# Optimization experiments

Hardware: AMD Instinct MI355X
Metric: run time of the kernel (lower is better)

Reference implementation:

```python
import jax, jax.numpy as jnp
import numpy as np
from math import gcd


def _get_start_index(length):
    if length <= 2:
        return 0
    return (length - 1) // 2


def setup_inputs() -> dict:
    key = jax.random.key(0)
    k1, k2 = jax.random.split(key)
    N = 8388608          # signal length (2^23 samples)
    F = 1023             # FIR taps
    x = jax.random.normal(k1, (N,), dtype=jnp.float32)
    filter_coeffs = jax.random.normal(k2, (F,), dtype=jnp.float32)
    return {"x": x, "up": 3, "down": 2, "filter_coeffs": filter_coeffs}


def reference(x, up, down, filter_coeffs):
    # Reduce the rational ratio (static Python ints)
    g = gcd(up, down)
    up = up // g
    down = down // g

    N = x.shape[0]
    F = filter_coeffs.shape[0]

    # Zero-stuff: x_up[::up] = up * x  -> length up*N
    x_up = jnp.zeros(up * N, dtype=x.dtype).at[::up].set(up * x)

    start = _get_start_index(F)
    out_len = (N * up) // down + bool((N * up) % down)

    if up == 1 and down == 1:
        return x_up[:out_len]

    # torch.conv1d(x_up, flip(h), padding=F-1) == full convolution np.convolve(x_up, h)
    full = jnp.convolve(x_up, filter_coeffs, mode="full")  # length up*N + F - 1
    x_out = full[start::down]
    return x_out[:out_len]
```

## Files before the change

### kernel.cpp

```cpp
#include <hip/hip_runtime.h>


typedef __attribute__((ext_vector_type(8))) short bf16x8;
typedef __attribute__((ext_vector_type(4))) float f32x4;

constexpr int SBLK = 4096;
constexpr int TPW  = 4;
constexpr int NQ   = 12;
constexpr int XSEG = 1072;
constexpr int AFN  = 3 * NQ * 64;

__device__ __forceinline__ unsigned short f2bf(float f) {
    union { float f; unsigned int u; } c; c.f = f;
    unsigned int u = c.u;
    return (unsigned short)((u + 0x7FFFu + ((u >> 16) & 1u)) >> 16);
}
__device__ __forceinline__ int swz(int seg) { return seg ^ ((seg >> 3) & 7); }

__global__ __launch_bounds__(256)
void build_afr_kernel(const float* __restrict__ h, uint4* __restrict__ afr)
{
    const int e = blockIdx.x * 256 + threadIdx.x;
    if (e >= AFN) return;
    const int r   = e / 768;
    const int rem = e - r * 768;
    const int q   = rem >> 6;
    const int le  = rem & 63;
    const int Tb  = 32 * q + 2 * (le & 15) + 8 * (le >> 4);
    unsigned int w[4];
    #pragma unroll
    for (int jp = 0; jp < 4; ++jp) {
        unsigned short half[2];
        #pragma unroll
        for (int u = 0; u < 2; ++u) {
            const int t   = Tb + 2 * jp + u - 32;
            const int hix = (r == 0) ? 3 * t - 2 : ((r == 1) ? 3 * t : 3 * t + 2);
            half[u] = (t >= 0 && hix >= 0 && hix < 1023) ? f2bf(3.0f * h[hix])
                                                         : (unsigned short)0;
        }
        w[jp] = (unsigned)half[0] | ((unsigned)half[1] << 16);
    }
    afr[e] = make_uint4(w[0], w[1], w[2], w[3]);
}

__global__ __launch_bounds__(256)
void resample_mfma_kernel(const float* __restrict__ x,
                          const uint4* __restrict__ afr,
                          float* __restrict__ out, int N)
{
    __shared__ __align__(16) unsigned short xr[8576];

    const int tid = threadIdx.x;
    const int s0  = blockIdx.x * SBLK;
    const int GHI = 2 * s0 + 8363;

    for (int st = tid; st < XSEG; st += 256) {
        const int g7 = GHI - 8 * st - 7;
        float f[8];
        if (g7 >= 0 && g7 + 7 < N) {
            const float4 lo = *reinterpret_cast<const float4*>(x + g7);
            const float4 hi = *reinterpret_cast<const float4*>(x + g7 + 4);
            f[0] = hi.w; f[1] = hi.z; f[2] = hi.y; f[3] = hi.x;
            f[4] = lo.w; f[5] = lo.z; f[6] = lo.y; f[7] = lo.x;
        } else {
            #pragma unroll
            for (int e = 0; e < 8; ++e) {
                const int idx = GHI - 8 * st - e;
                f[e] = (idx >= 0 && idx < N) ? x[idx] : 0.0f;
            }
        }
        uint4 w;
        w.x = (unsigned)f2bf(f[0]) | ((unsigned)f2bf(f[1]) << 16);
        w.y = (unsigned)f2bf(f[2]) | ((unsigned)f2bf(f[3]) << 16);
        w.z = (unsigned)f2bf(f[4]) | ((unsigned)f2bf(f[5]) << 16);
        w.w = (unsigned)f2bf(f[6]) | ((unsigned)f2bf(f[7]) << 16);
        *reinterpret_cast<uint4*>(xr + 8 * swz(st)) = w;
    }
    __syncthreads();

    const int wave = tid >> 6;
    const int lane = tid & 63;
    const int n    = lane & 15;
    const int quad = lane >> 4;

    f32x4 acc[TPW][3] = {};

    #pragma unroll 2
    for (int q = 0; q < NQ; ++q) {
        bf16x8 A[3];
        #pragma unroll
        for (int r = 0; r < 3; ++r)
            A[r] = __builtin_bit_cast(bf16x8, afr[(r * 12 + q) * 64 + lane]);
        #pragma unroll
        for (int jj = 0; jj < TPW; ++jj) {
            const int tile = wave * TPW + jj;
            const int seg  = 1020 - 64 * tile - 4 * n + 4 * q + quad;
            const bf16x8 B = __builtin_bit_cast(
                bf16x8, *reinterpret_cast<const uint4*>(xr + 8 * swz(seg)));
            #pragma unroll
            for (int r = 0; r < 3; ++r)
                acc[jj][r] = __builtin_amdgcn_mfma_f32_16x16x32_bf16(A[r], B, acc[jj][r], 0, 0, 0);
        }
    }

    #pragma unroll
    for (int jj = 0; jj < TPW; ++jj) {
        const int T = wave * TPW + jj;
        float v[12];
        #pragma unroll
        for (int r = 0; r < 3; ++r)
            #pragma unroll
            for (int i = 0; i < 4; ++i)
                v[3 * i + r] = acc[jj][r][i];
        float* po = out + 3 * s0 + 768 * T + 48 * n + 12 * quad;
        *reinterpret_cast<float4*>(po)     = make_float4(v[0], v[1], v[2],  v[3]);
        *reinterpret_cast<float4*>(po + 4) = make_float4(v[4], v[5], v[6],  v[7]);
        *reinterpret_cast<float4*>(po + 8) = make_float4(v[8], v[9], v[10], v[11]);
    }
}

extern "C" void kernel_launch(void* const* d_in, const int* in_sizes, int n_in,
                              void* d_out, int out_size, void* d_ws, size_t ws_size,
                              hipStream_t stream)
{
    const float* x = (const float*)d_in[0];
    const float* h = (const float*)d_in[3];
    float* out = (float*)d_out;
    uint4* afr = (uint4*)d_ws;

    const int N    = in_sizes[0];
    const int S    = out_size / 3;
    const int nblk = S / SBLK;

    build_afr_kernel<<<(AFN + 255) / 256, 256, 0, stream>>>(h, afr);
    resample_mfma_kernel<<<nblk, 256, 0, stream>>>(x, afr, out, N);
}
```

Before: 107.3 us.

## Switch polyphase FIR to 32x32x16 MFMA tiles with reordered LDS layout

Replaces the 16x16x32 bf16 MFMA formulation (four tiles per wave, 12 K-steps, three phases) with 32x32x16 MFMAs that accumulate 3 phase accumulators over 26 K-steps. The filter fragment table and the LDS signal layout are rebuilt to match, and the signal is stored in forward order. The float-to-bf16 packing moves to a cheaper round-half-up perm instruction, and launch bounds request 4 blocks per CU. This aims to cut LDS reads and MFMA issue overhead per output. The trade-offs are a slightly different bf16 rounding for x and heavier register pressure from the 16-wide accumulators.

New measurement: 113.5 us. +5.8%, slower.

```diff
diff --git a/kernel.cpp b/kernel.cpp
--- a/kernel.cpp
+++ b/kernel.cpp
@@ -1,19 +1,23 @@
 #include <hip/hip_runtime.h>
 
 
-typedef __attribute__((ext_vector_type(8))) short bf16x8;
-typedef __attribute__((ext_vector_type(4))) float f32x4;
+typedef __attribute__((ext_vector_type(8)))  short bf16x8;
+typedef __attribute__((ext_vector_type(16))) float f32x16;
 
-constexpr int SBLK = 4096;
-constexpr int TPW  = 4;
-constexpr int NQ   = 12;
-constexpr int XSEG = 1072;
-constexpr int AFN  = 3 * NQ * 64;
+constexpr int SBLK   = 4096;
+constexpr int NQ     = 26;
+constexpr int NGROUP = 1073;
+constexpr int LDSSEG = 1080;
+constexpr int AFE    = NQ * 192;
 
-__device__ __forceinline__ unsigned short f2bf(float f) {
-    union { float f; unsigned int u; } c; c.f = f;
-    unsigned int u = c.u;
-    return (unsigned short)((u + 0x7FFFu + ((u >> 16) & 1u)) >> 16);
+__device__ __forceinline__ unsigned short f2bf_rne(float f) {
+    union { float f; unsigned u; } c; c.f = f;
+    return (unsigned short)((c.u + 0x7FFFu + ((c.u >> 16) & 1u)) >> 16);
+}
+__device__ __forceinline__ unsigned pk2(float a, float b) {
+    unsigned ua = __builtin_bit_cast(unsigned, a) + 0x8000u;
+    unsigned ub = __builtin_bit_cast(unsigned, b) + 0x8000u;
+    return __builtin_amdgcn_perm(ub, ua, 0x07060302);
 }
 __device__ __forceinline__ int swz(int seg) { return seg ^ ((seg >> 3) & 7); }
 
@@ -21,101 +25,102 @@
 void build_afr_kernel(const float* __restrict__ h, uint4* __restrict__ afr)
 {
     const int e = blockIdx.x * 256 + threadIdx.x;
-    if (e >= AFN) return;
-    const int r   = e / 768;
-    const int rem = e - r * 768;
-    const int q   = rem >> 6;
-    const int le  = rem & 63;
-    const int Tb  = 32 * q + 2 * (le & 15) + 8 * (le >> 4);
-    unsigned int w[4];
+    if (e >= AFE) return;
+    const int qq   = e / 192;
+    const int rem  = e - qq * 192;
+    const int r    = rem >> 6;
+    const int lane = rem & 63;
+    const int m    = lane & 31;
+    const int hh   = lane >> 5;
+    const int ub   = 16 * (qq + 2) - 2 * m + 8 * hh;
+    unsigned w[4];
     #pragma unroll
     for (int jp = 0; jp < 4; ++jp) {
         unsigned short half[2];
         #pragma unroll
-        for (int u = 0; u < 2; ++u) {
-            const int t   = Tb + 2 * jp + u - 32;
+        for (int uu = 0; uu < 2; ++uu) {
+            const int u   = ub + 2 * jp + uu;
+            const int t   = 381 - u;
             const int hix = (r == 0) ? 3 * t - 2 : ((r == 1) ? 3 * t : 3 * t + 2);
-            half[u] = (t >= 0 && hix >= 0 && hix < 1023) ? f2bf(3.0f * h[hix])
-                                                         : (unsigned short)0;
+            half[uu] = (t >= 0 && hix >= 0 && hix < 1023) ? f2bf_rne(3.0f * h[hix])
+                                                          : (unsigned short)0;
         }
         w[jp] = (unsigned)half[0] | ((unsigned)half[1] << 16);
     }
     afr[e] = make_uint4(w[0], w[1], w[2], w[3]);
 }
 
-__global__ __launch_bounds__(256)
+__global__ __launch_bounds__(256, 4)
 void resample_mfma_kernel(const float* __restrict__ x,
                           const uint4* __restrict__ afr,
                           float* __restrict__ out, int N)
 {
-    __shared__ __align__(16) unsigned short xr[8576];
+    __shared__ __align__(16) unsigned short xb[LDSSEG * 8];
 
     const int tid = threadIdx.x;
     const int s0  = blockIdx.x * SBLK;
-    const int GHI = 2 * s0 + 8363;
+    const int A0  = 2 * s0 - 212;
+    char* lb = (char*)xb;
 
-    for (int st = tid; st < XSEG; st += 256) {
-        const int g7 = GHI - 8 * st - 7;
+    for (int it = 0; it < 5; ++it) {
+        const int g = tid + 256 * it;
+        if (g >= NGROUP) break;
+        const int gb = A0 + 8 * g;
         float f[8];
-        if (g7 >= 0 && g7 + 7 < N) {
-            const float4 lo = *reinterpret_cast<const float4*>(x + g7);
-            const float4 hi = *reinterpret_cast<const float4*>(x + g7 + 4);
-            f[0] = hi.w; f[1] = hi.z; f[2] = hi.y; f[3] = hi.x;
-            f[4] = lo.w; f[5] = lo.z; f[6] = lo.y; f[7] = lo.x;
+        if (gb >= 0 && gb + 7 < N) {
+            const float4 lo = *reinterpret_cast<const float4*>(x + gb);
+            const float4 hi = *reinterpret_cast<const float4*>(x + gb + 4);
+            f[0]=lo.x; f[1]=lo.y; f[2]=lo.z; f[3]=lo.w;
+            f[4]=hi.x; f[5]=hi.y; f[6]=hi.z; f[7]=hi.w;
         } else {
             #pragma unroll
             for (int e = 0; e < 8; ++e) {
-                const int idx = GHI - 8 * st - e;
+                const int idx = gb + e;
                 f[e] = (idx >= 0 && idx < N) ? x[idx] : 0.0f;
             }
         }
-        uint4 w;
-        w.x = (unsigned)f2bf(f[0]) | ((unsigned)f2bf(f[1]) << 16);
-        w.y = (unsigned)f2bf(f[2]) | ((unsigned)f2bf(f[3]) << 16);
-        w.z = (unsigned)f2bf(f[4]) | ((unsigned)f2bf(f[5]) << 16);
-        w.w = (unsigned)f2bf(f[6]) | ((unsigned)f2bf(f[7]) << 16);
-        *reinterpret_cast<uint4*>(xr + 8 * swz(st)) = w;
+        const unsigned p01 = pk2(f[0], f[1]);
+        const unsigned p23 = pk2(f[2], f[3]);
+        const unsigned p45 = pk2(f[4], f[5]);
+        const unsigned p67 = pk2(f[6], f[7]);
+        *reinterpret_cast<unsigned*>(lb + 16 * swz(g) + 12)    = p01;
+        *reinterpret_cast<uint2*>  (lb + 16 * swz(g + 1))      = make_uint2(p23, p45);
+        *reinterpret_cast<unsigned*>(lb + 16 * swz(g + 1) + 8) = p67;
     }
     __syncthreads();
 
     const int wave = tid >> 6;
     const int lane = tid & 63;
-    const int n    = lane & 15;
-    const int quad = lane >> 4;
+    const int n    = lane & 31;
+    const int hh   = lane >> 5;
 
-    f32x4 acc[TPW][3] = {};
+    f32x16 acc[3] = {};
 
-    #pragma unroll 2
-    for (int q = 0; q < NQ; ++q) {
-        bf16x8 A[3];
+    const int segbase = 256 * wave + 8 * n + hh + 1;
+    const uint4* ap = afr + lane;
+
+    #pragma unroll
+    for (int qq = 0; qq < NQ; ++qq) {
+        const int seg = segbase + 2 * (qq + 2);
+        const bf16x8 B = __builtin_bit_cast(
+            bf16x8, *reinterpret_cast<const uint4*>(lb + 16 * swz(seg)));
         #pragma unroll
-        for (int r = 0; r < 3; ++r)
-            A[r] = __builtin_bit_cast(bf16x8, afr[(r * 12 + q) * 64 + lane]);
-        #pragma unroll
-        for (int jj = 0; jj < TPW; ++jj) {
-            const int tile = wave * TPW + jj;
-            const int seg  = 1020 - 64 * tile - 4 * n + 4 * q + quad;
-            const bf16x8 B = __builtin_bit_cast(
-                bf16x8, *reinterpret_cast<const uint4*>(xr + 8 * swz(seg)));
-            #pragma unroll
-            for (int r = 0; r < 3; ++r)
-                acc[jj][r] = __builtin_amdgcn_mfma_f32_16x16x32_bf16(A[r], B, acc[jj][r], 0, 0, 0);
+        for (int r = 0; r < 3; ++r) {
+            const bf16x8 A = __builtin_bit_cast(bf16x8, ap[qq * 192 + r * 64]);
+            acc[r] = __builtin_amdgcn_mfma_f32_32x32x16_bf16(A, B, acc[r], 0, 0, 0);
         }
     }
 
+    float* ob = out + 3 * s0 + 3072 * wave + 12 * hh + 96 * n;
     #pragma unroll
-    for (int jj = 0; jj < TPW; ++jj) {
-        const int T = wave * TPW + jj;
-        float v[12];
-        #pragma unroll
-        for (int r = 0; r < 3; ++r)
-            #pragma unroll
-            for (int i = 0; i < 4; ++i)
-                v[3 * i + r] = acc[jj][r][i];
-        float* po = out + 3 * s0 + 768 * T + 48 * n + 12 * quad;
-        *reinterpret_cast<float4*>(po)     = make_float4(v[0], v[1], v[2],  v[3]);
-        *reinterpret_cast<float4*>(po + 4) = make_float4(v[4], v[5], v[6],  v[7]);
-        *reinterpret_cast<float4*>(po + 8) = make_float4(v[8], v[9], v[10], v[11]);
+    for (int c = 0; c < 4; ++c) {
+        float* p = ob + 24 * c;
+        *reinterpret_cast<float4*>(p) =
+            make_float4(acc[0][4*c],   acc[1][4*c],   acc[2][4*c],   acc[0][4*c+1]);
+        *reinterpret_cast<float4*>(p + 4) =
+            make_float4(acc[1][4*c+1], acc[2][4*c+1], acc[0][4*c+2], acc[1][4*c+2]);
+        *reinterpret_cast<float4*>(p + 8) =
+            make_float4(acc[2][4*c+2], acc[0][4*c+3], acc[1][4*c+3], acc[2][4*c+3]);
     }
 }
 
@@ -132,6 +137,6 @@
     const int S    = out_size / 3;
     const int nblk = S / SBLK;
 
-    build_afr_kernel<<<(AFN + 255) / 256, 256, 0, stream>>>(h, afr);
+    build_afr_kernel<<<(AFE + 255) / 256, 256, 0, stream>>>(h, afr);
     resample_mfma_kernel<<<nblk, 256, 0, stream>>>(x, afr, out, N);
 }
```
